# Performance work log

Hardware: AMD Instinct MI355X
Metric: run time of the kernel (lower is better)

The kernel has to match this reference:

```python
import jax, jax.numpy as jnp
import numpy as np

N_NODES = 100000


def _gcn_layer(x, W, b, src, dst, n):
    """PyG GCNConv: out = D^-1/2 (A+I) D^-1/2 (x W) + b, edge-list form.
    src/dst already include self-loops."""
    xw = x @ W                                        # [N, F_out]
    deg = jax.ops.segment_sum(jnp.ones_like(dst, dtype=xw.dtype), dst,
                              num_segments=n)         # in-degree incl. self-loops
    dinv = jnp.where(deg > 0, jax.lax.rsqrt(deg), 0.0)
    norm = dinv[src] * dinv[dst]                      # [E]
    msgs = norm[:, None] * xw[src]                    # gather + scale
    out = jax.ops.segment_sum(msgs, dst, num_segments=n)  # scatter-add
    return out + b


def _with_self_loops(edge_index, n):
    loops = jnp.arange(n, dtype=edge_index.dtype)
    src = jnp.concatenate([edge_index[0], loops])
    dst = jnp.concatenate([edge_index[1], loops])
    return src, dst


def setup_inputs() -> dict:
    key = jax.random.key(0)
    ks = jax.random.split(key, 10)
    n, f = N_NODES, 128
    e = 1_600_000
    ep = 500_000
    def glorot(k, shape):
        lim = np.sqrt(6.0 / (shape[0] + shape[1]))
        return jax.random.uniform(k, shape, jnp.float32, -lim, lim)
    return {
        "x": jax.random.normal(ks[0], (n, f), jnp.float32),
        "train_pos_edge_index": jax.random.randint(ks[1], (2, e), 0, n),
        "pos_edge_index": jax.random.randint(ks[2], (2, ep), 0, n),
        "neg_edge_index": jax.random.randint(ks[3], (2, ep), 0, n),
        "W1": glorot(ks[4], (f, 128)), "b1": jnp.zeros((128,), jnp.float32),
        "W2": glorot(ks[5], (128, 64)), "b2": jnp.zeros((64,), jnp.float32),
        "W3": glorot(ks[6], (64, 64)), "b3": jnp.zeros((64,), jnp.float32),
    }


def reference(x, train_pos_edge_index, pos_edge_index, neg_edge_index,
              W1, b1, W2, b2, W3, b3):
    n = x.shape[0]
    src, dst = _with_self_loops(train_pos_edge_index, n)
    h = jax.nn.relu(_gcn_layer(x, W1, b1, src, dst, n))
    h = jax.nn.relu(_gcn_layer(h, W2, b2, src, dst, n))
    embed = h
    h = _gcn_layer(h, W3, b3, src, dst, n)
    total = jnp.concatenate([pos_edge_index, neg_edge_index], axis=-1)  # [2, Ep+En]
    x_j = h[total[0]]
    x_i = h[total[1]]
    scores = jnp.einsum("ef,ef->e", x_i, x_j)
    return scores, embed
```

## Files before the change

kernel.cpp:

```cpp
#include <hip/hip_runtime.h>
#include <hip/hip_bf16.h>


#define ECH 4096
#define SHIFT 8
#define MAXNB 512

typedef __attribute__((ext_vector_type(8))) short bf16x8;
typedef __attribute__((ext_vector_type(4))) float f32x4;

__device__ __forceinline__ float lo16f(uint32_t u) { uint32_t x = u << 16; float f; __builtin_memcpy(&f, &x, 4); return f; }
__device__ __forceinline__ float hi16f(uint32_t u) { uint32_t x = u & 0xffff0000u; float f; __builtin_memcpy(&f, &x, 4); return f; }
__device__ __forceinline__ float u16f(unsigned short u) { uint32_t x = (uint32_t)u << 16; float f; __builtin_memcpy(&f, &x, 4); return f; }
__device__ __forceinline__ uint32_t pk2(float a, float b) {
    union { __hip_bfloat162 h; uint32_t u; } cv;
    cv.h = __hip_bfloat162(__float2bfloat16(a), __float2bfloat16(b));
    return cv.u;
}
__device__ __forceinline__ unsigned short bf16bits(float a) {
    union { __hip_bfloat16 b; unsigned short u; } cv;
    cv.b = __float2bfloat16(a);
    return cv.u;
}
__device__ __forceinline__ int pad8(int c) { return (c + 7) & ~7; }

__global__ __launch_bounds__(256) void part_hist_kernel(const int* __restrict__ dst, int E,
                                                        int B, int NB, int* __restrict__ histG) {
    __shared__ int h[MAXNB];
    int t = threadIdx.x, blk = blockIdx.x;
    for (int i = t; i < NB; i += 256) h[i] = 0;
    __syncthreads();
    int lo = blk * ECH, hi = min(lo + ECH, E);
    for (int i = lo + t; i < hi; i += 256) atomicAdd(&h[dst[i] >> SHIFT], 1);
    __syncthreads();
    for (int k = t; k < NB; k += 256) histG[(size_t)k * B + blk] = h[k];
}

__global__ __launch_bounds__(256) void part_scan_kernel(int* __restrict__ histG, int B,
                                                        int* __restrict__ bucketTotal) {
    __shared__ int sc[1024];
    int k = blockIdx.x, t = threadIdx.x;
    for (int i = t; i < 1024; i += 256) sc[i] = (i < B) ? histG[(size_t)k * B + i] : 0;
    __syncthreads();
    for (int o = 1; o < 1024; o <<= 1) {
        int v[4];
#pragma unroll
        for (int j = 0; j < 4; ++j) { int i = t + j * 256; v[j] = (i >= o) ? sc[i - o] : 0; }
        __syncthreads();
#pragma unroll
        for (int j = 0; j < 4; ++j) sc[t + j * 256] += v[j];
        __syncthreads();
    }
    for (int i = t; i < B; i += 256) histG[(size_t)k * B + i] = (i > 0) ? sc[i - 1] : 0;
    if (t == 0) bucketTotal[k] = sc[B - 1];
}

__global__ __launch_bounds__(256) void bucket_base_kernel(const int* __restrict__ bucketTotal,
                                                          int NB, int* __restrict__ bucketBase) {
    __shared__ int sc[MAXNB];
    int t = threadIdx.x;
    for (int i = t; i < MAXNB; i += 256) sc[i] = (i < NB) ? bucketTotal[i] : 0;
    __syncthreads();
    for (int o = 1; o < MAXNB; o <<= 1) {
        int v[MAXNB / 256];
#pragma unroll
        for (int j = 0; j < MAXNB / 256; ++j) { int i = t + j * 256; v[j] = (i >= o) ? sc[i - o] : 0; }
        __syncthreads();
#pragma unroll
        for (int j = 0; j < MAXNB / 256; ++j) sc[t + j * 256] += v[j];
        __syncthreads();
    }
    for (int i = t; i < NB; i += 256) bucketBase[i] = (i > 0) ? sc[i - 1] : 0;
}

__global__ __launch_bounds__(256) void part_scatter_kernel(
    const int* __restrict__ src, const int* __restrict__ dst, int E, int B, int NB,
    const int* __restrict__ histG, const int* __restrict__ bucketBase,
    int2* __restrict__ bedges) {
    __shared__ int cur[MAXNB];
    int t = threadIdx.x, blk = blockIdx.x;
    for (int k = t; k < NB; k += 256) cur[k] = bucketBase[k] + histG[(size_t)k * B + blk];
    __syncthreads();
    int lo = blk * ECH, hi = min(lo + ECH, E);
    for (int i = lo + t; i < hi; i += 256) {
        int s = src[i], d = dst[i];
        int p = atomicAdd(&cur[d >> SHIFT], 1);
        bedges[p] = make_int2(s, d);
    }
}

__global__ __launch_bounds__(256) void count_bucket_kernel(
    const int2* __restrict__ bedges, const int* __restrict__ bucketBase,
    const int* __restrict__ bucketTotal, int n, int* __restrict__ count) {
    __shared__ int hist[1 << SHIFT];
    int k = blockIdx.x, t = threadIdx.x;
    hist[t] = 0;
    __syncthreads();
    int base = bucketBase[k], cnt = bucketTotal[k];
    int d0 = k << SHIFT;
    for (int i = t; i < cnt; i += 256) atomicAdd(&hist[bedges[base + i].y - d0], 1);
    __syncthreads();
    int d = d0 + t;
    if (d < n) count[d] = hist[t];
}

__global__ __launch_bounds__(256) void scan_partial_kernel(const int* __restrict__ count, int n,
                                                           int* __restrict__ partial) {
    __shared__ int red[256];
    int t = threadIdx.x;
    int base = blockIdx.x * 1024 + t * 4;
    int s = 0;
#pragma unroll
    for (int i = 0; i < 4; ++i) {
        int idx = base + i;
        if (idx < n) s += pad8(count[idx]);
    }
    red[t] = s;
    __syncthreads();
    for (int o = 128; o > 0; o >>= 1) {
        if (t < o) red[t] += red[t + o];
        __syncthreads();
    }
    if (t == 0) partial[blockIdx.x] = red[0];
}

__global__ __launch_bounds__(256) void scan_offsets_kernel(int* __restrict__ partial, int nb,
                                                           int* __restrict__ row_ptr, int n) {
    __shared__ int sc[256];
    int t = threadIdx.x;
    sc[t] = (t < nb) ? partial[t] : 0;
    __syncthreads();
    for (int o = 1; o < 256; o <<= 1) {
        int v = sc[t];
        int u = (t >= o) ? sc[t - o] : 0;
        __syncthreads();
        sc[t] = v + u;
        __syncthreads();
    }
    if (t < nb) partial[t] = (t > 0) ? sc[t - 1] : 0;
    if (t == 0) row_ptr[n] = sc[255];
}

__global__ __launch_bounds__(256) void scan_write_kernel(const int* __restrict__ count, int n,
                                                         const int* __restrict__ partial,
                                                         int* __restrict__ row_ptr,
                                                         float* __restrict__ dinv) {
    __shared__ int sc[256];
    int t = threadIdx.x;
    int base = blockIdx.x * 1024 + t * 4;
    int c[4];
    int s = 0;
#pragma unroll
    for (int i = 0; i < 4; ++i) {
        int idx = base + i;
        c[i] = (idx < n) ? count[idx] : 0;
        s += pad8(c[i]);
    }
    sc[t] = s;
    __syncthreads();
    for (int o = 1; o < 256; o <<= 1) {
        int v = sc[t];
        int u = (t >= o) ? sc[t - o] : 0;
        __syncthreads();
        sc[t] = v + u;
        __syncthreads();
    }
    int run = partial[blockIdx.x] + ((t > 0) ? sc[t - 1] : 0);
#pragma unroll
    for (int i = 0; i < 4; ++i) {
        int idx = base + i;
        if (idx < n) {
            row_ptr[idx] = run;
            dinv[idx] = rsqrtf((float)c[i] + 1.0f);
            run += pad8(c[i]);
        }
    }
}

__global__ __launch_bounds__(256) void csr_fill_kernel(
    const int2* __restrict__ bedges, const int* __restrict__ bucketBase,
    const int* __restrict__ bucketTotal, const int* __restrict__ row_ptr,
    const float* __restrict__ dinv, int n, int2* __restrict__ colw) {
    __shared__ int cur[1 << SHIFT];
    int k = blockIdx.x, t = threadIdx.x;
    int d0 = k << SHIFT;
    for (int i = t; i < (1 << SHIFT); i += 256) {
        int d = d0 + i;
        cur[i] = (d < n) ? row_ptr[d] : 0;
    }
    __syncthreads();
    int base = bucketBase[k], cnt = bucketTotal[k];
    for (int i = t; i < cnt; i += 256) {
        int2 e = bedges[base + i];
        float w = dinv[e.x];
        int p = atomicAdd(&cur[e.y - d0], 1);
        colw[p] = make_int2(e.x, __float_as_int(w));
    }
    __syncthreads();
    for (int i = t; i < (1 << SHIFT); i += 256) {
        int d = d0 + i;
        if (d < n) {
            int pend = row_ptr[d + 1];
            for (int p = cur[i]; p < pend; ++p) colw[p] = make_int2(d, 0);
        }
    }
}

template<int K, int N>
__global__ __launch_bounds__(256) void packW_kernel(const float* __restrict__ W,
                                                    __hip_bfloat16* __restrict__ Wp) {
    constexpr int NT = N / 16;
    int idx = blockIdx.x * 256 + threadIdx.x;
    if (idx >= (K / 32) * NT * 64) return;
    int lane = idx & 63;
    int ct = (idx >> 6) % NT;
    int kc = idx / (64 * NT);
    int col = ct * 16 + (lane & 15);
    int k0 = kc * 32 + (lane >> 4) * 8;
    unsigned short tmp[8];
#pragma unroll
    for (int j = 0; j < 8; ++j) tmp[j] = bf16bits(W[(size_t)(k0 + j) * N + col]);
    ((uint4*)Wp)[idx] = *(const uint4*)tmp;
}

__global__ __launch_bounds__(256) void gemm1_mfma_kernel(
    const float* __restrict__ In, const __hip_bfloat16* __restrict__ Wp,
    __hip_bfloat16* __restrict__ Out, int n) {
    __shared__ unsigned short sA[64 * 40];
    int t = threadIdx.x;
    int wv = t >> 6, lane = t & 63;
    int rbase = blockIdx.x * 64;
    f32x4 acc[8] = {};
    int srow = t >> 2;
    int kseg = (t & 3) * 8;
    int arow = wv * 16 + (lane & 15);
    int aoff = (lane >> 4) * 8;
    for (int kc = 0; kc < 4; ++kc) {
        {
            int gr = rbase + srow;
            unsigned short tmp[8];
            if (gr < n) {
                const float* src = &In[(size_t)gr * 128 + kc * 32 + kseg];
                float4 v0 = *(const float4*)src;
                float4 v1 = *(const float4*)(src + 4);
                tmp[0] = bf16bits(v0.x); tmp[1] = bf16bits(v0.y);
                tmp[2] = bf16bits(v0.z); tmp[3] = bf16bits(v0.w);
                tmp[4] = bf16bits(v1.x); tmp[5] = bf16bits(v1.y);
                tmp[6] = bf16bits(v1.z); tmp[7] = bf16bits(v1.w);
            } else {
#pragma unroll
                for (int j = 0; j < 8; ++j) tmp[j] = 0;
            }
            *(uint4*)&sA[srow * 40 + kseg] = *(const uint4*)tmp;
        }
        __syncthreads();
        bf16x8 afrag = *(const bf16x8*)&sA[arow * 40 + aoff];
        const uint4* wp = (const uint4*)Wp + (size_t)kc * 512 + lane;
#pragma unroll
        for (int ct = 0; ct < 8; ++ct) {
            uint4 braw = wp[ct * 64];
            bf16x8 bfrag;
            __builtin_memcpy(&bfrag, &braw, 16);
            acc[ct] = __builtin_amdgcn_mfma_f32_16x16x32_bf16(afrag, bfrag, acc[ct], 0, 0, 0);
        }
        __syncthreads();
    }
    int orow0 = rbase + wv * 16 + (lane >> 4) * 4;
    int ocol = lane & 15;
#pragma unroll
    for (int ct = 0; ct < 8; ++ct) {
#pragma unroll
        for (int r = 0; r < 4; ++r) {
            int gr = orow0 + r;
            if (gr < n)
                ((unsigned short*)Out)[(size_t)gr * 128 + ct * 16 + ocol] = bf16bits(acc[ct][r]);
        }
    }
}

__global__ __launch_bounds__(256) void gemmA_mfma_kernel(
    const __hip_bfloat16* __restrict__ In, const __hip_bfloat16* __restrict__ Wp,
    __hip_bfloat16* __restrict__ Out, int n) {
    int t = threadIdx.x;
    int wv = t >> 6, lane = t & 63;
    int rbase = blockIdx.x * 64 + wv * 16;
    int arow = rbase + (lane & 15);
    bool rowok = (arow < n);
    f32x4 acc[4] = {};
    const unsigned short* a_base = (const unsigned short*)In + (size_t)(rowok ? arow : 0) * 128 + (lane >> 4) * 8;
#pragma unroll
    for (int kc = 0; kc < 4; ++kc) {
        bf16x8 afrag = {};
        if (rowok) {
            uint4 araw = *(const uint4*)(a_base + kc * 32);
            __builtin_memcpy(&afrag, &araw, 16);
        }
        const uint4* wp = (const uint4*)Wp + (size_t)kc * 256 + lane;
#pragma unroll
        for (int ct = 0; ct < 4; ++ct) {
            uint4 braw = wp[ct * 64];
            bf16x8 bfrag;
            __builtin_memcpy(&bfrag, &braw, 16);
            acc[ct] = __builtin_amdgcn_mfma_f32_16x16x32_bf16(afrag, bfrag, acc[ct], 0, 0, 0);
        }
    }
    int orow0 = rbase + (lane >> 4) * 4;
    int ocol = lane & 15;
#pragma unroll
    for (int ct = 0; ct < 4; ++ct) {
#pragma unroll
        for (int r = 0; r < 4; ++r) {
            int gr = orow0 + r;
            if (gr < n)
                ((unsigned short*)Out)[(size_t)gr * 64 + ct * 16 + ocol] = bf16bits(acc[ct][r]);
        }
    }
}

__global__ __launch_bounds__(256) void gemmB_mfma_kernel(
    const float* __restrict__ In, const __hip_bfloat16* __restrict__ Wp,
    __hip_bfloat16* __restrict__ Out, int n) {
    int t = threadIdx.x;
    int wv = t >> 6, lane = t & 63;
    int rbase = blockIdx.x * 64 + wv * 16;
    int arow = rbase + (lane & 15);
    bool rowok = (arow < n);
    f32x4 acc[4] = {};
    const float* a_base = In + (size_t)(rowok ? arow : 0) * 64 + (lane >> 4) * 8;
#pragma unroll
    for (int kc = 0; kc < 2; ++kc) {
        bf16x8 afrag = {};
        if (rowok) {
            float4 v0 = *(const float4*)(a_base + kc * 32);
            float4 v1 = *(const float4*)(a_base + kc * 32 + 4);
            unsigned short tmp[8];
            tmp[0] = bf16bits(v0.x); tmp[1] = bf16bits(v0.y);
            tmp[2] = bf16bits(v0.z); tmp[3] = bf16bits(v0.w);
            tmp[4] = bf16bits(v1.x); tmp[5] = bf16bits(v1.y);
            tmp[6] = bf16bits(v1.z); tmp[7] = bf16bits(v1.w);
            __builtin_memcpy(&afrag, tmp, 16);
        }
        const uint4* wp = (const uint4*)Wp + (size_t)kc * 256 + lane;
#pragma unroll
        for (int ct = 0; ct < 4; ++ct) {
            uint4 braw = wp[ct * 64];
            bf16x8 bfrag;
            __builtin_memcpy(&bfrag, &braw, 16);
            acc[ct] = __builtin_amdgcn_mfma_f32_16x16x32_bf16(afrag, bfrag, acc[ct], 0, 0, 0);
        }
    }
    int orow0 = rbase + (lane >> 4) * 4;
    int ocol = lane & 15;
#pragma unroll
    for (int ct = 0; ct < 4; ++ct) {
#pragma unroll
        for (int r = 0; r < 4; ++r) {
            int gr = orow0 + r;
            if (gr < n)
                ((unsigned short*)Out)[(size_t)gr * 64 + ct * 16 + ocol] = bf16bits(acc[ct][r]);
        }
    }
}

__global__ __launch_bounds__(256) void gather128_kernel(
    const __hip_bfloat16* __restrict__ xw, const int* __restrict__ row_ptr,
    const int2* __restrict__ colw, const float* __restrict__ dinv,
    const float* __restrict__ b1, __hip_bfloat16* __restrict__ h1, int n) {
    int w = threadIdx.x >> 6, l = threadIdx.x & 63;
    int d = blockIdx.x * 4 + w;
    if (d >= n) return;
    float dd = dinv[d];
    int p0 = __builtin_amdgcn_readfirstlane(row_ptr[d]);
    int p1 = __builtin_amdgcn_readfirstlane(row_ptr[d + 1]);
    const uint32_t* X = (const uint32_t*)xw;
    uint32_t v = X[(size_t)d * 64 + l];
    float a0 = dd * lo16f(v), a1 = dd * hi16f(v);
    float c0a = 0.f, c1a = 0.f;
    for (int e = p0; e < p1; e += 8) {
        int s0 = __builtin_amdgcn_readfirstlane(colw[e].x);
        int s1 = __builtin_amdgcn_readfirstlane(colw[e + 1].x);
        int s2 = __builtin_amdgcn_readfirstlane(colw[e + 2].x);
        int s3 = __builtin_amdgcn_readfirstlane(colw[e + 3].x);
        int s4 = __builtin_amdgcn_readfirstlane(colw[e + 4].x);
        int s5 = __builtin_amdgcn_readfirstlane(colw[e + 5].x);
        int s6 = __builtin_amdgcn_readfirstlane(colw[e + 6].x);
        int s7 = __builtin_amdgcn_readfirstlane(colw[e + 7].x);
        float w0 = __int_as_float(__builtin_amdgcn_readfirstlane(colw[e].y));
        float w1 = __int_as_float(__builtin_amdgcn_readfirstlane(colw[e + 1].y));
        float w2 = __int_as_float(__builtin_amdgcn_readfirstlane(colw[e + 2].y));
        float w3 = __int_as_float(__builtin_amdgcn_readfirstlane(colw[e + 3].y));
        float w4 = __int_as_float(__builtin_amdgcn_readfirstlane(colw[e + 4].y));
        float w5 = __int_as_float(__builtin_amdgcn_readfirstlane(colw[e + 5].y));
        float w6 = __int_as_float(__builtin_amdgcn_readfirstlane(colw[e + 6].y));
        float w7 = __int_as_float(__builtin_amdgcn_readfirstlane(colw[e + 7].y));
        uint32_t v0 = X[(size_t)s0 * 64 + l];
        uint32_t v1 = X[(size_t)s1 * 64 + l];
        uint32_t v2 = X[(size_t)s2 * 64 + l];
        uint32_t v3 = X[(size_t)s3 * 64 + l];
        uint32_t v4 = X[(size_t)s4 * 64 + l];
        uint32_t v5 = X[(size_t)s5 * 64 + l];
        uint32_t v6 = X[(size_t)s6 * 64 + l];
        uint32_t v7 = X[(size_t)s7 * 64 + l];
        a0 = fmaf(w0, lo16f(v0), a0);  a1 = fmaf(w0, hi16f(v0), a1);
        c0a = fmaf(w1, lo16f(v1), c0a); c1a = fmaf(w1, hi16f(v1), c1a);
        a0 = fmaf(w2, lo16f(v2), a0);  a1 = fmaf(w2, hi16f(v2), a1);
        c0a = fmaf(w3, lo16f(v3), c0a); c1a = fmaf(w3, hi16f(v3), c1a);
        a0 = fmaf(w4, lo16f(v4), a0);  a1 = fmaf(w4, hi16f(v4), a1);
        c0a = fmaf(w5, lo16f(v5), c0a); c1a = fmaf(w5, hi16f(v5), c1a);
        a0 = fmaf(w6, lo16f(v6), a0);  a1 = fmaf(w6, hi16f(v6), a1);
        c0a = fmaf(w7, lo16f(v7), c0a); c1a = fmaf(w7, hi16f(v7), c1a);
    }
    a0 += c0a; a1 += c1a;
    a0 = fmaxf(fmaf(dd, a0, b1[2 * l]), 0.0f);
    a1 = fmaxf(fmaf(dd, a1, b1[2 * l + 1]), 0.0f);
    ((uint32_t*)h1)[(size_t)d * 64 + l] = pk2(a0, a1);
}

template<bool RELU, int OUT>
__global__ __launch_bounds__(256) void gather64b_kernel(
    const __hip_bfloat16* __restrict__ xw, const int* __restrict__ row_ptr,
    const int2* __restrict__ colw, const float* __restrict__ dinv,
    const float* __restrict__ b, void* __restrict__ out, int n) {
    int w = threadIdx.x >> 6, l = threadIdx.x & 63;
    int d = blockIdx.x * 4 + w;
    if (d >= n) return;
    float dd = dinv[d];
    int p0 = __builtin_amdgcn_readfirstlane(row_ptr[d]);
    int p1 = __builtin_amdgcn_readfirstlane(row_ptr[d + 1]);
    const unsigned short* X = (const unsigned short*)xw;
    float a = dd * u16f(X[(size_t)d * 64 + l]);
    float c = 0.f;
    for (int e = p0; e < p1; e += 8) {
        int s0 = __builtin_amdgcn_readfirstlane(colw[e].x);
        int s1 = __builtin_amdgcn_readfirstlane(colw[e + 1].x);
        int s2 = __builtin_amdgcn_readfirstlane(colw[e + 2].x);
        int s3 = __builtin_amdgcn_readfirstlane(colw[e + 3].x);
        int s4 = __builtin_amdgcn_readfirstlane(colw[e + 4].x);
        int s5 = __builtin_amdgcn_readfirstlane(colw[e + 5].x);
        int s6 = __builtin_amdgcn_readfirstlane(colw[e + 6].x);
        int s7 = __builtin_amdgcn_readfirstlane(colw[e + 7].x);
        float w0 = __int_as_float(__builtin_amdgcn_readfirstlane(colw[e].y));
        float w1 = __int_as_float(__builtin_amdgcn_readfirstlane(colw[e + 1].y));
        float w2 = __int_as_float(__builtin_amdgcn_readfirstlane(colw[e + 2].y));
        float w3 = __int_as_float(__builtin_amdgcn_readfirstlane(colw[e + 3].y));
        float w4 = __int_as_float(__builtin_amdgcn_readfirstlane(colw[e + 4].y));
        float w5 = __int_as_float(__builtin_amdgcn_readfirstlane(colw[e + 5].y));
        float w6 = __int_as_float(__builtin_amdgcn_readfirstlane(colw[e + 6].y));
        float w7 = __int_as_float(__builtin_amdgcn_readfirstlane(colw[e + 7].y));
        unsigned short v0 = X[(size_t)s0 * 64 + l];
        unsigned short v1 = X[(size_t)s1 * 64 + l];
        unsigned short v2 = X[(size_t)s2 * 64 + l];
        unsigned short v3 = X[(size_t)s3 * 64 + l];
        unsigned short v4 = X[(size_t)s4 * 64 + l];
        unsigned short v5 = X[(size_t)s5 * 64 + l];
        unsigned short v6 = X[(size_t)s6 * 64 + l];
        unsigned short v7 = X[(size_t)s7 * 64 + l];
        a = fmaf(w0, u16f(v0), a);
        c = fmaf(w1, u16f(v1), c);
        a = fmaf(w2, u16f(v2), a);
        c = fmaf(w3, u16f(v3), c);
        a = fmaf(w4, u16f(v4), a);
        c = fmaf(w5, u16f(v5), c);
        a = fmaf(w6, u16f(v6), a);
        c = fmaf(w7, u16f(v7), c);
    }
    a += c;
    float r = fmaf(dd, a, b[l]);
    if (RELU) r = fmaxf(r, 0.0f);
    if (OUT == 0) ((float*)out)[(size_t)d * 64 + l] = r;
    else ((unsigned short*)out)[(size_t)d * 64 + l] = bf16bits(r);
}

__global__ void score_kernel(const __hip_bfloat16* __restrict__ h, const int* __restrict__ pos,
                             const int* __restrict__ neg, int Ep, int En,
                             float* __restrict__ out) {
    int wid = (int)(((size_t)blockIdx.x * blockDim.x + threadIdx.x) >> 6);
    int lane = threadIdx.x & 63;
    int g = lane >> 3, sl = lane & 7;
    int ed = wid * 8 + g;
    int tot = Ep + En;
    if (ed >= tot) return;
    int j, i;
    if (ed < Ep) { j = pos[ed]; i = pos[Ep + ed]; }
    else { int e = ed - Ep; j = neg[e]; i = neg[En + e]; }
    const uint4* X = (const uint4*)h;
    uint4 vi = X[(size_t)i * 8 + sl];
    uint4 vj = X[(size_t)j * 8 + sl];
    float v;
    v = lo16f(vi.x) * lo16f(vj.x);
    v = fmaf(hi16f(vi.x), hi16f(vj.x), v);
    v = fmaf(lo16f(vi.y), lo16f(vj.y), v);
    v = fmaf(hi16f(vi.y), hi16f(vj.y), v);
    v = fmaf(lo16f(vi.z), lo16f(vj.z), v);
    v = fmaf(hi16f(vi.z), hi16f(vj.z), v);
    v = fmaf(lo16f(vi.w), lo16f(vj.w), v);
    v = fmaf(hi16f(vi.w), hi16f(vj.w), v);
#pragma unroll
    for (int o = 4; o > 0; o >>= 1) v += __shfl_xor(v, o);
    if (sl == 0) out[ed] = v;
}

extern "C" void kernel_launch(void* const* d_in, const int* in_sizes, int n_in,
                              void* d_out, int out_size, void* d_ws, size_t ws_size,
                              hipStream_t stream) {
    const float* x   = (const float*)d_in[0];
    const int* train = (const int*)d_in[1];
    const int* pos   = (const int*)d_in[2];
    const int* neg   = (const int*)d_in[3];
    const float* W1  = (const float*)d_in[4];
    const float* b1  = (const float*)d_in[5];
    const float* W2  = (const float*)d_in[6];
    const float* b2  = (const float*)d_in[7];
    const float* W3  = (const float*)d_in[8];
    const float* b3  = (const float*)d_in[9];

    const int n  = in_sizes[0] / 128;
    const int E  = in_sizes[1] / 2;
    const int Ep = in_sizes[2] / 2;
    const int En = in_sizes[3] / 2;

    const int B  = (E + ECH - 1) / ECH;
    const int NB = ((n - 1) >> SHIFT) + 1;

    char* wp = (char*)d_ws;
    auto alloc = [&](size_t bytes) { char* r = wp; wp += (bytes + 255) & ~(size_t)255; return r; };
    int*   count    = (int*)alloc((size_t)n * 4);
    int*   row_ptr  = (int*)alloc(((size_t)n + 1) * 4);
    int*   partial  = (int*)alloc(256 * 4);
    int*   bucketTotal = (int*)alloc(MAXNB * 4);
    int*   bucketBase  = (int*)alloc(MAXNB * 4);
    __hip_bfloat16* Wp1 = (__hip_bfloat16*)alloc(4 * 8 * 64 * 8 * 2);
    __hip_bfloat16* Wp2 = (__hip_bfloat16*)alloc(4 * 4 * 64 * 8 * 2);
    __hip_bfloat16* Wp3 = (__hip_bfloat16*)alloc(2 * 4 * 64 * 8 * 2);
    int2*  colw     = (int2*)alloc(((size_t)E + 8 * (size_t)n) * 8);
    float* dinv     = (float*)alloc((size_t)n * 4);
    __hip_bfloat16* xw1 = (__hip_bfloat16*)alloc((size_t)n * 128 * 2);
    __hip_bfloat16* h1  = (__hip_bfloat16*)alloc((size_t)n * 128 * 2);
    __hip_bfloat16* P   = (__hip_bfloat16*)alloc((size_t)n * 64 * 2);
    __hip_bfloat16* h3  = xw1;
    __hip_bfloat16* xw3 = P;
    int2* bedges = (int2*)h1;
    int*  histG  = (int*)P;

    float* out_scores = (float*)d_out;
    float* out_embed  = out_scores + (Ep + En);

    const int nbs = (n + 1023) / 1024;

    part_hist_kernel<<<B, 256, 0, stream>>>(train + E, E, B, NB, histG);
    part_scan_kernel<<<NB, 256, 0, stream>>>(histG, B, bucketTotal);
    bucket_base_kernel<<<1, 256, 0, stream>>>(bucketTotal, NB, bucketBase);
    part_scatter_kernel<<<B, 256, 0, stream>>>(train, train + E, E, B, NB, histG, bucketBase, bedges);
    count_bucket_kernel<<<NB, 256, 0, stream>>>(bedges, bucketBase, bucketTotal, n, count);
    scan_partial_kernel<<<nbs, 256, 0, stream>>>(count, n, partial);
    scan_offsets_kernel<<<1, 256, 0, stream>>>(partial, nbs, row_ptr, n);
    scan_write_kernel<<<nbs, 256, 0, stream>>>(count, n, partial, row_ptr, dinv);
    csr_fill_kernel<<<NB, 256, 0, stream>>>(bedges, bucketBase, bucketTotal, row_ptr, dinv, n, colw);

    packW_kernel<128, 128><<<8, 256, 0, stream>>>(W1, Wp1);
    packW_kernel<128, 64><<<4, 256, 0, stream>>>(W2, Wp2);
    packW_kernel<64, 64><<<2, 256, 0, stream>>>(W3, Wp3);

    gemm1_mfma_kernel<<<(n + 63) / 64, 256, 0, stream>>>(x, Wp1, xw1, n);
    gather128_kernel<<<(n + 3) / 4, 256, 0, stream>>>(xw1, row_ptr, colw, dinv, b1, h1, n);
    gemmA_mfma_kernel<<<(n + 63) / 64, 256, 0, stream>>>(h1, Wp2, P, n);

    gather64b_kernel<true, 0><<<(n + 3) / 4, 256, 0, stream>>>(
        P, row_ptr, colw, dinv, b2, out_embed, n);

    gemmB_mfma_kernel<<<(n + 63) / 64, 256, 0, stream>>>(out_embed, Wp3, xw3, n);
    gather64b_kernel<false, 1><<<(n + 3) / 4, 256, 0, stream>>>(
        xw3, row_ptr, colw, dinv, b3, h3, n);

    {
        int waves = (Ep + En + 7) / 8;
        score_kernel<<<(int)(((size_t)waves * 64 + 255) / 256), 256, 0, stream>>>(
            h3, pos, neg, Ep, En, out_scores);
    }
}
```

Before: 293.5 us.

## Pack bucketed edges and CSR entries into 32-bit words with quantized weights

```diff
diff --git a/kernel.cpp b/kernel.cpp
--- a/kernel.cpp
+++ b/kernel.cpp
@@ -23,6 +23,7 @@
     return cv.u;
 }
 __device__ __forceinline__ int pad8(int c) { return (c + 7) & ~7; }
+#define WDEC (1.0f / 32767.0f)
 
 __global__ __launch_bounds__(256) void part_hist_kernel(const int* __restrict__ dst, int E,
                                                         int B, int NB, int* __restrict__ histG) {
@@ -76,7 +77,7 @@
 __global__ __launch_bounds__(256) void part_scatter_kernel(
     const int* __restrict__ src, const int* __restrict__ dst, int E, int B, int NB,
     const int* __restrict__ histG, const int* __restrict__ bucketBase,
-    int2* __restrict__ bedges) {
+    uint32_t* __restrict__ bedges) {
     __shared__ int cur[MAXNB];
     int t = threadIdx.x, blk = blockIdx.x;
     for (int k = t; k < NB; k += 256) cur[k] = bucketBase[k] + histG[(size_t)k * B + blk];
@@ -85,22 +86,21 @@
     for (int i = lo + t; i < hi; i += 256) {
         int s = src[i], d = dst[i];
         int p = atomicAdd(&cur[d >> SHIFT], 1);
-        bedges[p] = make_int2(s, d);
+        bedges[p] = ((uint32_t)s << 8) | (uint32_t)(d & 255);
     }
 }
 
 __global__ __launch_bounds__(256) void count_bucket_kernel(
-    const int2* __restrict__ bedges, const int* __restrict__ bucketBase,
+    const uint32_t* __restrict__ bedges, const int* __restrict__ bucketBase,
     const int* __restrict__ bucketTotal, int n, int* __restrict__ count) {
     __shared__ int hist[1 << SHIFT];
     int k = blockIdx.x, t = threadIdx.x;
     hist[t] = 0;
     __syncthreads();
     int base = bucketBase[k], cnt = bucketTotal[k];
-    int d0 = k << SHIFT;
-    for (int i = t; i < cnt; i += 256) atomicAdd(&hist[bedges[base + i].y - d0], 1);
-    __syncthreads();
-    int d = d0 + t;
+    for (int i = t; i < cnt; i += 256) atomicAdd(&hist[bedges[base + i] & 255u], 1);
+    __syncthreads();
+    int d = (k << SHIFT) + t;
     if (d < n) count[d] = hist[t];
 }
 
@@ -178,9 +178,9 @@
 }
 
 __global__ __launch_bounds__(256) void csr_fill_kernel(
-    const int2* __restrict__ bedges, const int* __restrict__ bucketBase,
+    const uint32_t* __restrict__ bedges, const int* __restrict__ bucketBase,
     const int* __restrict__ bucketTotal, const int* __restrict__ row_ptr,
-    const float* __restrict__ dinv, int n, int2* __restrict__ colw) {
+    const float* __restrict__ dinv, int n, uint32_t* __restrict__ colw) {
     __shared__ int cur[1 << SHIFT];
     int k = blockIdx.x, t = threadIdx.x;
     int d0 = k << SHIFT;
@@ -191,17 +191,19 @@
     __syncthreads();
     int base = bucketBase[k], cnt = bucketTotal[k];
     for (int i = t; i < cnt; i += 256) {
-        int2 e = bedges[base + i];
-        float w = dinv[e.x];
-        int p = atomicAdd(&cur[e.y - d0], 1);
-        colw[p] = make_int2(e.x, __float_as_int(w));
+        uint32_t e = bedges[base + i];
+        int s = (int)(e >> 8);
+        uint32_t wq = (uint32_t)(dinv[s] * 32767.0f + 0.5f);
+        int p = atomicAdd(&cur[e & 255u], 1);
+        colw[p] = ((uint32_t)s << 15) | wq;
     }
     __syncthreads();
     for (int i = t; i < (1 << SHIFT); i += 256) {
         int d = d0 + i;
         if (d < n) {
             int pend = row_ptr[d + 1];
-            for (int p = cur[i]; p < pend; ++p) colw[p] = make_int2(d, 0);
+            uint32_t padv = (uint32_t)d << 15;
+            for (int p = cur[i]; p < pend; ++p) colw[p] = padv;
         }
     }
 }
@@ -255,10 +257,10 @@
         }
         __syncthreads();
         bf16x8 afrag = *(const bf16x8*)&sA[arow * 40 + aoff];
-        const uint4* wp = (const uint4*)Wp + (size_t)kc * 512 + lane;
+        const uint4* wpp = (const uint4*)Wp + (size_t)kc * 512 + lane;
 #pragma unroll
         for (int ct = 0; ct < 8; ++ct) {
-            uint4 braw = wp[ct * 64];
+            uint4 braw = wpp[ct * 64];
             bf16x8 bfrag;
             __builtin_memcpy(&bfrag, &braw, 16);
             acc[ct] = __builtin_amdgcn_mfma_f32_16x16x32_bf16(afrag, bfrag, acc[ct], 0, 0, 0);
@@ -295,10 +297,10 @@
             uint4 araw = *(const uint4*)(a_base + kc * 32);
             __builtin_memcpy(&afrag, &araw, 16);
         }
-        const uint4* wp = (const uint4*)Wp + (size_t)kc * 256 + lane;
+        const uint4* wpp = (const uint4*)Wp + (size_t)kc * 256 + lane;
 #pragma unroll
         for (int ct = 0; ct < 4; ++ct) {
-            uint4 braw = wp[ct * 64];
+            uint4 braw = wpp[ct * 64];
             bf16x8 bfrag;
             __builtin_memcpy(&bfrag, &braw, 16);
             acc[ct] = __builtin_amdgcn_mfma_f32_16x16x32_bf16(afrag, bfrag, acc[ct], 0, 0, 0);
@@ -340,10 +342,10 @@
             tmp[6] = bf16bits(v1.z); tmp[7] = bf16bits(v1.w);
             __builtin_memcpy(&afrag, tmp, 16);
         }
-        const uint4* wp = (const uint4*)Wp + (size_t)kc * 256 + lane;
+        const uint4* wpp = (const uint4*)Wp + (size_t)kc * 256 + lane;
 #pragma unroll
         for (int ct = 0; ct < 4; ++ct) {
-            uint4 braw = wp[ct * 64];
+            uint4 braw = wpp[ct * 64];
             bf16x8 bfrag;
             __builtin_memcpy(&bfrag, &braw, 16);
             acc[ct] = __builtin_amdgcn_mfma_f32_16x16x32_bf16(afrag, bfrag, acc[ct], 0, 0, 0);
@@ -362,9 +364,11 @@
     }
 }
 
+#define DECODE(q, s, w) int s = (int)((q) >> 15); float w = (float)((q) & 0x7fffu) * WDEC;
+
 __global__ __launch_bounds__(256) void gather128_kernel(
     const __hip_bfloat16* __restrict__ xw, const int* __restrict__ row_ptr,
-    const int2* __restrict__ colw, const float* __restrict__ dinv,
+    const uint32_t* __restrict__ colw, const float* __restrict__ dinv,
     const float* __restrict__ b1, __hip_bfloat16* __restrict__ h1, int n) {
     int w = threadIdx.x >> 6, l = threadIdx.x & 63;
     int d = blockIdx.x * 4 + w;
@@ -377,22 +381,16 @@
     float a0 = dd * lo16f(v), a1 = dd * hi16f(v);
     float c0a = 0.f, c1a = 0.f;
     for (int e = p0; e < p1; e += 8) {
-        int s0 = __builtin_amdgcn_readfirstlane(colw[e].x);
-        int s1 = __builtin_amdgcn_readfirstlane(colw[e + 1].x);
-        int s2 = __builtin_amdgcn_readfirstlane(colw[e + 2].x);
-        int s3 = __builtin_amdgcn_readfirstlane(colw[e + 3].x);
-        int s4 = __builtin_amdgcn_readfirstlane(colw[e + 4].x);
-        int s5 = __builtin_amdgcn_readfirstlane(colw[e + 5].x);
-        int s6 = __builtin_amdgcn_readfirstlane(colw[e + 6].x);
-        int s7 = __builtin_amdgcn_readfirstlane(colw[e + 7].x);
-        float w0 = __int_as_float(__builtin_amdgcn_readfirstlane(colw[e].y));
-        float w1 = __int_as_float(__builtin_amdgcn_readfirstlane(colw[e + 1].y));
-        float w2 = __int_as_float(__builtin_amdgcn_readfirstlane(colw[e + 2].y));
-        float w3 = __int_as_float(__builtin_amdgcn_readfirstlane(colw[e + 3].y));
-        float w4 = __int_as_float(__builtin_amdgcn_readfirstlane(colw[e + 4].y));
-        float w5 = __int_as_float(__builtin_amdgcn_readfirstlane(colw[e + 5].y));
-        float w6 = __int_as_float(__builtin_amdgcn_readfirstlane(colw[e + 6].y));
-        float w7 = __int_as_float(__builtin_amdgcn_readfirstlane(colw[e + 7].y));
+        uint32_t q0 = __builtin_amdgcn_readfirstlane(colw[e]);
+        uint32_t q1 = __builtin_amdgcn_readfirstlane(colw[e + 1]);
+        uint32_t q2 = __builtin_amdgcn_readfirstlane(colw[e + 2]);
+        uint32_t q3 = __builtin_amdgcn_readfirstlane(colw[e + 3]);
+        uint32_t q4 = __builtin_amdgcn_readfirstlane(colw[e + 4]);
+        uint32_t q5 = __builtin_amdgcn_readfirstlane(colw[e + 5]);
+        uint32_t q6 = __builtin_amdgcn_readfirstlane(colw[e + 6]);
+        uint32_t q7 = __builtin_amdgcn_readfirstlane(colw[e + 7]);
+        DECODE(q0, s0, w0) DECODE(q1, s1, w1) DECODE(q2, s2, w2) DECODE(q3, s3, w3)
+        DECODE(q4, s4, w4) DECODE(q5, s5, w5) DECODE(q6, s6, w6) DECODE(q7, s7, w7)
         uint32_t v0 = X[(size_t)s0 * 64 + l];
         uint32_t v1 = X[(size_t)s1 * 64 + l];
         uint32_t v2 = X[(size_t)s2 * 64 + l];
@@ -419,7 +417,7 @@
 template<bool RELU, int OUT>
 __global__ __launch_bounds__(256) void gather64b_kernel(
     const __hip_bfloat16* __restrict__ xw, const int* __restrict__ row_ptr,
-    const int2* __restrict__ colw, const float* __restrict__ dinv,
+    const uint32_t* __restrict__ colw, const float* __restrict__ dinv,
     const float* __restrict__ b, void* __restrict__ out, int n) {
     int w = threadIdx.x >> 6, l = threadIdx.x & 63;
     int d = blockIdx.x * 4 + w;
@@ -431,22 +429,16 @@
     float a = dd * u16f(X[(size_t)d * 64 + l]);
     float c = 0.f;
     for (int e = p0; e < p1; e += 8) {
-        int s0 = __builtin_amdgcn_readfirstlane(colw[e].x);
-        int s1 = __builtin_amdgcn_readfirstlane(colw[e + 1].x);
-        int s2 = __builtin_amdgcn_readfirstlane(colw[e + 2].x);
-        int s3 = __builtin_amdgcn_readfirstlane(colw[e + 3].x);
-        int s4 = __builtin_amdgcn_readfirstlane(colw[e + 4].x);
-        int s5 = __builtin_amdgcn_readfirstlane(colw[e + 5].x);
-        int s6 = __builtin_amdgcn_readfirstlane(colw[e + 6].x);
-        int s7 = __builtin_amdgcn_readfirstlane(colw[e + 7].x);
-        float w0 = __int_as_float(__builtin_amdgcn_readfirstlane(colw[e].y));
-        float w1 = __int_as_float(__builtin_amdgcn_readfirstlane(colw[e + 1].y));
-        float w2 = __int_as_float(__builtin_amdgcn_readfirstlane(colw[e + 2].y));
-        float w3 = __int_as_float(__builtin_amdgcn_readfirstlane(colw[e + 3].y));
-        float w4 = __int_as_float(__builtin_amdgcn_readfirstlane(colw[e + 4].y));
-        float w5 = __int_as_float(__builtin_amdgcn_readfirstlane(colw[e + 5].y));
-        float w6 = __int_as_float(__builtin_amdgcn_readfirstlane(colw[e + 6].y));
-        float w7 = __int_as_float(__builtin_amdgcn_readfirstlane(colw[e + 7].y));
+        uint32_t q0 = __builtin_amdgcn_readfirstlane(colw[e]);
+        uint32_t q1 = __builtin_amdgcn_readfirstlane(colw[e + 1]);
+        uint32_t q2 = __builtin_amdgcn_readfirstlane(colw[e + 2]);
+        uint32_t q3 = __builtin_amdgcn_readfirstlane(colw[e + 3]);
+        uint32_t q4 = __builtin_amdgcn_readfirstlane(colw[e + 4]);
+        uint32_t q5 = __builtin_amdgcn_readfirstlane(colw[e + 5]);
+        uint32_t q6 = __builtin_amdgcn_readfirstlane(colw[e + 6]);
+        uint32_t q7 = __builtin_amdgcn_readfirstlane(colw[e + 7]);
+        DECODE(q0, s0, w0) DECODE(q1, s1, w1) DECODE(q2, s2, w2) DECODE(q3, s3, w3)
+        DECODE(q4, s4, w4) DECODE(q5, s5, w5) DECODE(q6, s6, w6) DECODE(q7, s7, w7)
         unsigned short v0 = X[(size_t)s0 * 64 + l];
         unsigned short v1 = X[(size_t)s1 * 64 + l];
         unsigned short v2 = X[(size_t)s2 * 64 + l];
@@ -532,14 +524,14 @@
     __hip_bfloat16* Wp1 = (__hip_bfloat16*)alloc(4 * 8 * 64 * 8 * 2);
     __hip_bfloat16* Wp2 = (__hip_bfloat16*)alloc(4 * 4 * 64 * 8 * 2);
     __hip_bfloat16* Wp3 = (__hip_bfloat16*)alloc(2 * 4 * 64 * 8 * 2);
-    int2*  colw     = (int2*)alloc(((size_t)E + 8 * (size_t)n) * 8);
+    uint32_t* colw  = (uint32_t*)alloc(((size_t)E + 8 * (size_t)n) * 4);
     float* dinv     = (float*)alloc((size_t)n * 4);
     __hip_bfloat16* xw1 = (__hip_bfloat16*)alloc((size_t)n * 128 * 2);
     __hip_bfloat16* h1  = (__hip_bfloat16*)alloc((size_t)n * 128 * 2);
     __hip_bfloat16* P   = (__hip_bfloat16*)alloc((size_t)n * 64 * 2);
     __hip_bfloat16* h3  = xw1;
     __hip_bfloat16* xw3 = P;
-    int2* bedges = (int2*)h1;
+    uint32_t* bedges = (uint32_t*)h1;
     int*  histG  = (int*)P;
 
     float* out_scores = (float*)d_out;
```

After: 280.1 us. -4.6%, faster.
